# Kernel tuning notes

Measured on AMD Instinct MI355X. Metric: run time of the kernel, lower is better.

Reference implementation:

```python
import jax, jax.numpy as jnp
import numpy as np

N = 200000          # number of nodes (objects)
H = 64              # hidden_size
ARITIES = [1, 2, 3] # arity per relation
NTUP = [250000, 250000, 250000]  # ground atoms per relation


def setup_inputs() -> dict:
    key = jax.random.key(0)
    ks = jax.random.split(key, 32)
    inp = {"node_states": jax.random.normal(ks[0], (N, H), jnp.float32)}
    i = 1
    for r, (a, t) in enumerate(zip(ARITIES, NTUP)):
        inp[f"rel{r}_idx"] = jax.random.randint(ks[i], (t * a,), 0, N, dtype=jnp.int32).astype(jnp.int64); i += 1
        d = a * H
        s = (2.0 / d) ** 0.5
        inp[f"w1_r{r}"] = jax.random.normal(ks[i], (d, d), jnp.float32) * s; i += 1
        inp[f"b1_r{r}"] = jnp.zeros((d,), jnp.float32)
        inp[f"w2_r{r}"] = jax.random.normal(ks[i], (d, d), jnp.float32) * s; i += 1
        inp[f"b2_r{r}"] = jnp.zeros((d,), jnp.float32)
    su = (1.0 / (2 * H)) ** 0.5
    inp["wu1"] = jax.random.normal(ks[i], (2 * H, 2 * H), jnp.float32) * su; i += 1
    inp["bu1"] = jnp.zeros((2 * H,), jnp.float32)
    inp["wu2"] = jax.random.normal(ks[i], (2 * H, H), jnp.float32) * su
    inp["bu2"] = jnp.zeros((H,), jnp.float32)
    return inp


def reference(node_states, rel0_idx, rel1_idx, rel2_idx,
              w1_r0, b1_r0, w2_r0, b2_r0,
              w1_r1, b1_r1, w2_r1, b2_r1,
              w1_r2, b1_r2, w2_r2, b2_r2,
              wu1, bu1, wu2, bu2):
    sum_msg = jnp.zeros_like(node_states)
    rels = [(ARITIES[0], rel0_idx, w1_r0, b1_r0, w2_r0, b2_r0),
            (ARITIES[1], rel1_idx, w1_r1, b1_r1, w2_r1, b2_r1),
            (ARITIES[2], rel2_idx, w1_r2, b1_r2, w2_r2, b2_r2)]
    for a, idx, w1, b1, w2, b2 in rels:
        # gather node states for each ground atom: [T, a*H]
        x = node_states[idx].reshape(-1, a * H)
        h = jax.nn.relu(x @ w1 + b1)
        msg = (h @ w2 + b2).reshape(-1, H)  # [T*a, H]
        # scatter-add messages back to their nodes
        sum_msg = sum_msg.at[idx].add(msg)
    z = jnp.concatenate([sum_msg, node_states], axis=1)  # [N, 2H]
    return jax.nn.relu(z @ wu1 + bu1) @ wu2 + bu2
```

## Files before the change

kernel.cpp:

```cpp
#include <hip/hip_runtime.h>

#define H 64

typedef __attribute__((ext_vector_type(8))) __bf16 bf16x8;
typedef __attribute__((ext_vector_type(4))) float f32x4;
typedef unsigned short u16;
typedef unsigned int u32;

union F8 { bf16x8 b; u16 u[8]; uint4 q; };

__device__ __forceinline__ u16 f2bf(float f) {
    union { __bf16 h; u16 u; } v; v.h = (__bf16)f; return v.u;
}
__device__ __forceinline__ float bf2f(u16 x) {
    return __uint_as_float((u32)x << 16);
}
__device__ __forceinline__ unsigned swz(int col, int k, int K) {
    return ((unsigned)(col * K + k) * 2u) ^ (((unsigned)col & 7u) << 4);
}

struct Seg { const float* src; unsigned dstBytes; int K; int N; };
struct Segs { Seg s[8]; };

__global__ __launch_bounds__(256) void conv_weights(Segs segs, char* out) {
    Seg sg = segs.s[blockIdx.y];
    int total = sg.K * sg.N;
    char* dst = out + sg.dstBytes;
    for (int e = blockIdx.x * 256 + threadIdx.x; e < total; e += gridDim.x * 256) {
        int k = e / sg.N, n = e % sg.N;
        *(u16*)(dst + swz(n, k, sg.K)) = f2bf(sg.src[e]);
    }
}

struct Prep {
    const float4* src; ushort4* dst; int n4;
    const int* idx[3]; int m[3];
    u32* cnt; u32* pos;
};

__global__ __launch_bounds__(256) void conv_nodes_rank(Prep a) {
    const int M01   = a.m[0] + a.m[1];
    const int total = a.n4 + M01 + a.m[2];
    for (int e = blockIdx.x * 256 + threadIdx.x; e < total; e += gridDim.x * 256) {
        if (e < a.n4) {
            float4 f = a.src[e];
            ushort4 o;
            o.x = f2bf(f.x); o.y = f2bf(f.y); o.z = f2bf(f.z); o.w = f2bf(f.w);
            a.dst[e] = o;
        } else {
            const int m = e - a.n4;
            int lm = m, r = 0;
            if (lm >= a.m[0]) {
                lm -= a.m[0]; r = 1;
                if (lm >= a.m[1]) { lm -= a.m[1]; r = 2; }
            }
            a.pos[m] = atomicAdd(a.cnt + a.idx[r][lm], 1u);
        }
    }
}

struct Fix { const int* idx[3]; int m[3]; const u32* base; u32* pos; };

__global__ __launch_bounds__(256) void rank_fix(Fix a) {
    const int total = a.m[0] + a.m[1] + a.m[2];
    for (int e = blockIdx.x * 256 + threadIdx.x; e < total; e += gridDim.x * 256) {
        int lm = e, r = 0;
        if (lm >= a.m[0]) {
            lm -= a.m[0]; r = 1;
            if (lm >= a.m[1]) { lm -= a.m[1]; r = 2; }
        }
        a.pos[e] += a.base[a.idx[r][lm]];
    }
}

__global__ __launch_bounds__(512) void scan_blocks(u32* __restrict__ data,
                                                   u32* __restrict__ sums, int n) {
    __shared__ u32 s[512];
    int tid = threadIdx.x, i = blockIdx.x * 512 + tid;
    u32 v = (i < n) ? data[i] : 0u;
    s[tid] = v; __syncthreads();
    for (int d = 1; d < 512; d <<= 1) {
        u32 t = (tid >= d) ? s[tid - d] : 0u; __syncthreads();
        s[tid] += t; __syncthreads();
    }
    if (i < n) data[i] = s[tid] - v;
    if (tid == 511) sums[blockIdx.x] = s[511];
}

__global__ __launch_bounds__(512) void scan_sums(u32* __restrict__ sums, int nb) {
    __shared__ u32 s[512];
    int tid = threadIdx.x;
    u32 v = (tid < nb) ? sums[tid] : 0u;
    s[tid] = v; __syncthreads();
    for (int d = 1; d < 512; d <<= 1) {
        u32 t = (tid >= d) ? s[tid - d] : 0u; __syncthreads();
        s[tid] += t; __syncthreads();
    }
    if (tid < nb) sums[tid] = s[tid] - v;
}

__global__ __launch_bounds__(512) void scan_add(u32* __restrict__ data,
                                                const u32* __restrict__ sums, int n) {
    int i = blockIdx.x * 512 + threadIdx.x;
    if (i < n) data[i] += sums[blockIdx.x];
}

template<int A>
__global__ __launch_bounds__(512, 4) void msg_kernel(
    const u16* __restrict__ nsb, const int* __restrict__ idx,
    const u32* __restrict__ pos,
    const u16* __restrict__ w1T, const float* __restrict__ b1,
    const u16* __restrict__ w2T, const float* __restrict__ b2,
    u16* __restrict__ msg, int T)
{
    constexpr int D   = A * 64;
    constexpr int KS  = D / 32;
    constexpr int NT  = D / 16;
    constexpr bool DUAL = (A == 1);
    constexpr int WH  = (A == 3) ? 3 : 1;
    constexpr int NTH = NT / WH;
    constexpr int COLH = D / WH;
    constexpr int NPF = (DUAL ? 2 * D * D : COLH * D) / 8 / 512;
    __shared__ __align__(16) u16 Wl[DUAL ? 2 * D * D : COLH * D];
    __shared__ __align__(16) u16 h1[128 * D];

    const int tid  = threadIdx.x;
    const int lane = tid & 63;
    const int w    = tid >> 6;
    const int g    = lane >> 4;
    const int lr   = lane & 15;

    const int tile = blockIdx.x * 128;
    const int trow = tile + w * 16 + lr;
    const int tl   = trow < T ? trow : T - 1;

    auto stage = [&](const u16* gsrc) {
#pragma unroll
        for (int i = 0; i < NPF; ++i) {
            const u16* gp = gsrc + ((i * 512 + tid) << 3);
            u16* lp = Wl + ((i * 512 + (w << 6)) << 3);
            __builtin_amdgcn_global_load_lds(
                (const __attribute__((address_space(1))) void*)gp,
                (__attribute__((address_space(3))) void*)lp, 16, 0, 0);
        }
    };

    int nodes[A];
#pragma unroll
    for (int s = 0; s < A; ++s) nodes[s] = idx[(long)tl * A + s];

    bf16x8 a1[KS];
#pragma unroll
    for (int kk = 0; kk < KS; ++kk) {
        const u16* p = nsb + (long)nodes[kk >> 1] * H + ((kk & 1) * 32 + g * 8);
        F8 t; t.q = *(const uint4*)p;
        a1[kk] = t.b;
    }

    float bias1[NT], bias2[NT];
#pragma unroll
    for (int j = 0; j < NT; ++j) bias1[j] = b1[j * 16 + lr];
#pragma unroll
    for (int j = 0; j < NT; ++j) bias2[j] = b2[j * 16 + lr];

#pragma unroll
    for (int hh = 0; hh < WH; ++hh) {
        stage(DUAL ? w1T : (w1T + (size_t)hh * COLH * D));
        asm volatile("s_waitcnt vmcnt(0)" ::: "memory");
        __syncthreads();

#pragma unroll
        for (int j = 0; j < NTH; ++j) {
            const int jg = hh * NTH + j;
            f32x4 acc = {0.f, 0.f, 0.f, 0.f};
#pragma unroll
            for (int kk = 0; kk < KS; ++kk) {
                F8 bf; bf.q = *(const uint4*)((const char*)Wl + swz(j * 16 + lr, kk * 32 + g * 8, D));
                acc = __builtin_amdgcn_mfma_f32_16x16x32_bf16(a1[kk], bf.b, acc, 0, 0, 0);
            }
#pragma unroll
            for (int r = 0; r < 4; ++r) {
                float vv = acc[r] + bias1[jg];
                vv = vv > 0.f ? vv : 0.f;
                int row = w * 16 + g * 4 + r;
                *(u16*)((char*)h1 + swz(row, jg * 16 + lr, D)) = f2bf(vv);
            }
        }
        if constexpr (!DUAL) __syncthreads();
    }

    bf16x8 a2[KS];
#pragma unroll
    for (int kk = 0; kk < KS; ++kk) {
        int row = w * 16 + lr;
        F8 t; t.q = *(const uint4*)((const char*)h1 + swz(row, kk * 32 + g * 8, D));
        a2[kk] = t.b;
    }

#pragma unroll
    for (int hh = 0; hh < WH; ++hh) {
        if constexpr (!DUAL) {
            stage(w2T + (size_t)hh * COLH * D);
            asm volatile("s_waitcnt vmcnt(0)" ::: "memory");
            __syncthreads();
        }
        const char* W2base = DUAL ? (const char*)(Wl + D * D) : (const char*)Wl;

#pragma unroll
        for (int j = 0; j < NTH; ++j) {
            const int jg = hh * NTH + j;
            f32x4 acc = {0.f, 0.f, 0.f, 0.f};
#pragma unroll
            for (int kk = 0; kk < KS; ++kk) {
                F8 bf; bf.q = *(const uint4*)(W2base + swz(j * 16 + lr, kk * 32 + g * 8, D));
                acc = __builtin_amdgcn_mfma_f32_16x16x32_bf16(a2[kk], bf.b, acc, 0, 0, 0);
            }
            const int gc   = jg * 16 + lr;
            const int slot = gc >> 6;
            const int cs   = gc & 63;
#pragma unroll
            for (int r = 0; r < 4; ++r) {
                int la   = w * 16 + g * 4 + r;
                int mrow = la * A + slot;
                unsigned byte = (((unsigned)(mrow * 64 + cs)) * 2u) ^ (((unsigned)mrow & 7u) << 4);
                *(u16*)((char*)h1 + byte) = f2bf(acc[r] + bias2[jg]);
            }
        }
        if constexpr (!DUAL) { if (hh + 1 < WH) __syncthreads(); }
    }

    const int  mbase = (tile + w * 16) * A;
    const bool full  = (tile + 128 <= T);
#pragma unroll
    for (int i = 0; i < 16 * A; i += 4) {
        int ml   = i + (lane >> 4);
        int mrow = w * 16 * A + ml;
        bool ok  = full || ((tile + w * 16 + ml / A) < T);
        if (ok) {
            u32 p = pos[mbase + ml];
            unsigned byte = (((unsigned)(mrow * 64 + (lane & 15) * 4)) * 2u) ^ (((unsigned)mrow & 7u) << 4);
            uint2 v = *(const uint2*)((const char*)h1 + byte);
            *(uint2*)(msg + (size_t)p * 64 + (lane & 15) * 4) = v;
        }
    }
}

template<int A, bool NSB>
__global__ __launch_bounds__(512) void rel_kernel(
    const float* __restrict__ ns, const u16* __restrict__ nsb,
    const int* __restrict__ idx,
    const u16* __restrict__ w1T, const float* __restrict__ b1,
    const u16* __restrict__ w2T, const float* __restrict__ b2,
    float* __restrict__ dout, int T)
{
    constexpr int D  = A * 64;
    constexpr int KS = D / 32;
    constexpr int NT = D / 16;
    constexpr bool DUAL = (A == 1);
    __shared__ __align__(16) u16 Wl[(DUAL ? 2 : 1) * D * D];
    __shared__ __align__(16) u16 h1[128 * D];

    const int tid  = threadIdx.x;
    const int lane = tid & 63;
    const int w    = tid >> 6;
    const int g    = lane >> 4;
    const int lr   = lane & 15;

    const int tile = blockIdx.x * 128;
    const int trow = tile + w * 16 + lr;
    const int tl   = trow < T ? trow : T - 1;

    {
        constexpr int NV = (DUAL ? 2 : 1) * D * D / 8;
        const uint4* s4 = (const uint4*)w1T;
        uint4* d4 = (uint4*)Wl;
#pragma unroll
        for (int i = 0; i < NV / 512; ++i) d4[i * 512 + tid] = s4[i * 512 + tid];
    }

    int nodes[A];
#pragma unroll
    for (int s = 0; s < A; ++s) nodes[s] = idx[(long)tl * A + s];

    bf16x8 a1[KS];
#pragma unroll
    for (int kk = 0; kk < KS; ++kk) {
        if constexpr (NSB) {
            const u16* p = nsb + (long)nodes[kk >> 1] * H + ((kk & 1) * 32 + g * 8);
            F8 t; t.q = *(const uint4*)p;
            a1[kk] = t.b;
        } else {
            const float* p = ns + (long)nodes[kk >> 1] * H + ((kk & 1) * 32 + g * 8);
            float4 f0 = *(const float4*)p;
            float4 f1 = *(const float4*)(p + 4);
            F8 t;
            t.u[0] = f2bf(f0.x); t.u[1] = f2bf(f0.y); t.u[2] = f2bf(f0.z); t.u[3] = f2bf(f0.w);
            t.u[4] = f2bf(f1.x); t.u[5] = f2bf(f1.y); t.u[6] = f2bf(f1.z); t.u[7] = f2bf(f1.w);
            a1[kk] = t.b;
        }
    }

    float bias1[NT];
#pragma unroll
    for (int j = 0; j < NT; ++j) bias1[j] = b1[j * 16 + lr];

    __syncthreads();

#pragma unroll
    for (int j = 0; j < NT; ++j) {
        f32x4 acc = {0.f, 0.f, 0.f, 0.f};
#pragma unroll
        for (int kk = 0; kk < KS; ++kk) {
            F8 bf; bf.q = *(const uint4*)((const char*)Wl + swz(j * 16 + lr, kk * 32 + g * 8, D));
            acc = __builtin_amdgcn_mfma_f32_16x16x32_bf16(a1[kk], bf.b, acc, 0, 0, 0);
        }
#pragma unroll
        for (int r = 0; r < 4; ++r) {
            float vv = acc[r] + bias1[j];
            vv = vv > 0.f ? vv : 0.f;
            int row = w * 16 + g * 4 + r;
            *(u16*)((char*)h1 + swz(row, j * 16 + lr, D)) = f2bf(vv);
        }
    }

    const char* W2base;
    if constexpr (!DUAL) {
        __syncthreads();
        const uint4* s4 = (const uint4*)w2T;
        uint4* d4 = (uint4*)Wl;
        constexpr int NV = D * D / 8;
#pragma unroll
        for (int i = 0; i < NV / 512; ++i) d4[i * 512 + tid] = s4[i * 512 + tid];
        W2base = (const char*)Wl;
    } else {
        W2base = (const char*)(Wl + D * D);
    }

    bf16x8 a2[KS];
#pragma unroll
    for (int kk = 0; kk < KS; ++kk) {
        int row = w * 16 + lr;
        F8 t; t.q = *(const uint4*)((const char*)h1 + swz(row, kk * 32 + g * 8, D));
        a2[kk] = t.b;
    }

    float bias2[NT];
#pragma unroll
    for (int j = 0; j < NT; ++j) bias2[j] = b2[j * 16 + lr];

    int  nodes2[A][4];
    bool pred[4];
#pragma unroll
    for (int r = 0; r < 4; ++r) {
        int t  = tile + w * 16 + g * 4 + r;
        int tc = t < T ? t : T - 1;
        pred[r] = t < T;
#pragma unroll
        for (int s = 0; s < A; ++s) nodes2[s][r] = idx[(long)tc * A + s];
    }
    if constexpr (!DUAL) __syncthreads();

#pragma unroll
    for (int j = 0; j < NT; ++j) {
        f32x4 acc = {0.f, 0.f, 0.f, 0.f};
#pragma unroll
        for (int kk = 0; kk < KS; ++kk) {
            F8 bf; bf.q = *(const uint4*)(W2base + swz(j * 16 + lr, kk * 32 + g * 8, D));
            acc = __builtin_amdgcn_mfma_f32_16x16x32_bf16(a2[kk], bf.b, acc, 0, 0, 0);
        }
        const int slot = j >> 2;
        const int coff = (j & 3) * 16 + lr;
#pragma unroll
        for (int r = 0; r < 4; ++r) {
            if (pred[r])
                unsafeAtomicAdd(dout + (long)nodes2[slot][r] * H + coff, acc[r] + bias2[j]);
        }
    }
}

template<bool SEG, bool NSB>
__global__ __launch_bounds__(512) void update_kernel(
    const float* __restrict__ ns, const u16* __restrict__ nsb,
    const float* __restrict__ sum,
    const u32* __restrict__ base, const u16* __restrict__ msg, int Mtot,
    const u16* __restrict__ wu1T, const float* __restrict__ bu1,
    const u16* __restrict__ wu2T, const float* __restrict__ bu2,
    float* __restrict__ out, int N)
{
    __shared__ __align__(16) u16 Wl[128 * 128 + 64 * 128];
    __shared__ __align__(16) u16 h[128 * 128];

    const int tid  = threadIdx.x;
    const int lane = tid & 63;
    const int w    = tid >> 6;
    const int g    = lane >> 4;
    const int lr   = lane & 15;

    {
        const uint4* s4 = (const uint4*)wu1T;
        uint4* d4 = (uint4*)Wl;
#pragma unroll
        for (int i = 0; i < 6; ++i) d4[i * 512 + tid] = s4[i * 512 + tid];
    }

    const int tile = blockIdx.x * 128;
    const int trow = tile + w * 16 + lr;
    const int tl   = trow < N ? trow : N - 1;

    bf16x8 a1[4];
    if constexpr (SEG) {
        const u32 s = base[tl];
        const u32 e = (tl + 1 < N) ? base[tl + 1] : (u32)Mtot;
        float s0[8], s1[8];
#pragma unroll
        for (int j = 0; j < 8; ++j) { s0[j] = 0.f; s1[j] = 0.f; }
        for (u32 p = s; p < e; ++p) {
            const u16* row = msg + (size_t)p * 64;
            F8 v0, v1;
            v0.q = *(const uint4*)(row + g * 8);
            v1.q = *(const uint4*)(row + 32 + g * 8);
#pragma unroll
            for (int j = 0; j < 8; ++j) { s0[j] += bf2f(v0.u[j]); s1[j] += bf2f(v1.u[j]); }
        }
        F8 t0, t1;
#pragma unroll
        for (int j = 0; j < 8; ++j) { t0.u[j] = f2bf(s0[j]); t1.u[j] = f2bf(s1[j]); }
        a1[0] = t0.b; a1[1] = t1.b;
    } else {
#pragma unroll
        for (int kk = 0; kk < 2; ++kk) {
            int k = kk * 32 + g * 8;
            const float* p = sum + (long)tl * H + k;
            float4 f0 = *(const float4*)p;
            float4 f1 = *(const float4*)(p + 4);
            F8 t;
            t.u[0] = f2bf(f0.x); t.u[1] = f2bf(f0.y); t.u[2] = f2bf(f0.z); t.u[3] = f2bf(f0.w);
            t.u[4] = f2bf(f1.x); t.u[5] = f2bf(f1.y); t.u[6] = f2bf(f1.z); t.u[7] = f2bf(f1.w);
            a1[kk] = t.b;
        }
    }
#pragma unroll
    for (int kk = 2; kk < 4; ++kk) {
        if (NSB) {
            const u16* prow = nsb + (long)tl * H;
            F8 t; t.q = *(const uint4*)(prow + (kk - 2) * 32 + g * 8);
            a1[kk] = t.b;
        } else {
            int k = (kk - 2) * 32 + g * 8;
            const float* p = ns + (long)tl * H + k;
            float4 f0 = *(const float4*)p;
            float4 f1 = *(const float4*)(p + 4);
            F8 t;
            t.u[0] = f2bf(f0.x); t.u[1] = f2bf(f0.y); t.u[2] = f2bf(f0.z); t.u[3] = f2bf(f0.w);
            t.u[4] = f2bf(f1.x); t.u[5] = f2bf(f1.y); t.u[6] = f2bf(f1.z); t.u[7] = f2bf(f1.w);
            a1[kk] = t.b;
        }
    }

    float bias1[8], bias2[4];
#pragma unroll
    for (int j = 0; j < 8; ++j) bias1[j] = bu1[j * 16 + lr];
#pragma unroll
    for (int j = 0; j < 4; ++j) bias2[j] = bu2[j * 16 + lr];

    __syncthreads();

#pragma unroll
    for (int j = 0; j < 8; ++j) {
        f32x4 acc = {0.f, 0.f, 0.f, 0.f};
#pragma unroll
        for (int kk = 0; kk < 4; ++kk) {
            F8 bf; bf.q = *(const uint4*)((const char*)Wl + swz(j * 16 + lr, kk * 32 + g * 8, 128));
            acc = __builtin_amdgcn_mfma_f32_16x16x32_bf16(a1[kk], bf.b, acc, 0, 0, 0);
        }
#pragma unroll
        for (int r = 0; r < 4; ++r) {
            float vv = acc[r] + bias1[j];
            vv = vv > 0.f ? vv : 0.f;
            int row = w * 16 + g * 4 + r;
            *(u16*)((char*)h + swz(row, j * 16 + lr, 128)) = f2bf(vv);
        }
    }

    bf16x8 a2[4];
#pragma unroll
    for (int kk = 0; kk < 4; ++kk) {
        int row = w * 16 + lr;
        F8 t; t.q = *(const uint4*)((const char*)h + swz(row, kk * 32 + g * 8, 128));
        a2[kk] = t.b;
    }

    const char* W2base = (const char*)(Wl + 128 * 128);
#pragma unroll
    for (int j = 0; j < 4; ++j) {
        f32x4 acc = {0.f, 0.f, 0.f, 0.f};
#pragma unroll
        for (int kk = 0; kk < 4; ++kk) {
            F8 bf; bf.q = *(const uint4*)(W2base + swz(j * 16 + lr, kk * 32 + g * 8, 128));
            acc = __builtin_amdgcn_mfma_f32_16x16x32_bf16(a2[kk], bf.b, acc, 0, 0, 0);
        }
#pragma unroll
        for (int r = 0; r < 4; ++r) {
            int t = tile + w * 16 + g * 4 + r;
            if (t < N) out[(long)t * H + j * 16 + lr] = acc[r] + bias2[j];
        }
    }
}

extern "C" void kernel_launch(void* const* d_in, const int* in_sizes, int n_in,
                              void* d_out, int out_size, void* d_ws, size_t ws_size,
                              hipStream_t stream) {
    const float* ns = (const float*)d_in[0];
    const int* idxs[3] = { (const int*)d_in[1], (const int*)d_in[6], (const int*)d_in[11] };
    const float* b1s[3] = { (const float*)d_in[3], (const float*)d_in[8], (const float*)d_in[13] };
    const float* b2s[3] = { (const float*)d_in[5], (const float*)d_in[10], (const float*)d_in[15] };
    const float* bu1 = (const float*)d_in[17];
    const float* bu2 = (const float*)d_in[19];

    const int N = in_sizes[0] / H;
    const int Ts[3] = { in_sizes[1], in_sizes[6] / 2, in_sizes[11] / 3 };
    const int Ms[3] = { Ts[0] * 1, Ts[1] * 2, Ts[2] * 3 };
    const long Mtot = (long)Ms[0] + Ms[1] + Ms[2];

    char* wsb = (char*)d_ws;
    auto AL = [](size_t x) { return (x + 255) & ~(size_t)255; };

    const unsigned O_W1R0 = 0;
    const unsigned O_W2R0 = O_W1R0 + 64 * 64 * 2;
    const unsigned O_W1R1 = O_W2R0 + 64 * 64 * 2;
    const unsigned O_W2R1 = O_W1R1 + 128 * 128 * 2;
    const unsigned O_W1R2 = O_W2R1 + 128 * 128 * 2;
    const unsigned O_W2R2 = O_W1R2 + 192 * 192 * 2;
    const unsigned O_WU1  = O_W2R2 + 192 * 192 * 2;
    const unsigned O_WU2  = O_WU1 + 128 * 128 * 2;
    const size_t  wEnd    = O_WU2 + 128 * 64 * 2;
    const unsigned wOff1[3] = { O_W1R0, O_W1R1, O_W1R2 };
    const unsigned wOff2[3] = { O_W2R0, O_W2R1, O_W2R2 };

    const int nb = (N + 511) / 512;

    const size_t O_CNT = AL(wEnd);
    const size_t O_SUM = AL(O_CNT + (size_t)N * 4);
    const size_t O_POS = AL(O_SUM + (size_t)nb * 4);
    const size_t O_NSB = AL(O_POS + (size_t)Mtot * 4);
    const size_t nsLen = (size_t)N * H * 2;
    const size_t O_MSG = AL(O_NSB + nsLen);
    const size_t need  = O_MSG + (size_t)Mtot * 128;

    const bool sorted = (nb <= 512) && (ws_size >= need);
    const bool nsbOk  = ws_size >= O_NSB + nsLen;

    Segs segs;
    segs.s[0] = {(const float*)d_in[2],  O_W1R0, 64, 64};
    segs.s[1] = {(const float*)d_in[4],  O_W2R0, 64, 64};
    segs.s[2] = {(const float*)d_in[7],  O_W1R1, 128, 128};
    segs.s[3] = {(const float*)d_in[9],  O_W2R1, 128, 128};
    segs.s[4] = {(const float*)d_in[12], O_W1R2, 192, 192};
    segs.s[5] = {(const float*)d_in[14], O_W2R2, 192, 192};
    segs.s[6] = {(const float*)d_in[16], O_WU1, 128, 128};
    segs.s[7] = {(const float*)d_in[18], O_WU2, 128, 64};

    conv_weights<<<dim3(36, 8), 256, 0, stream>>>(segs, wsb);

    float* dout = (float*)d_out;
    u16* nsbp = (u16*)(wsb + O_NSB);

    const u16* W1[3] = { (const u16*)(wsb + wOff1[0]), (const u16*)(wsb + wOff1[1]), (const u16*)(wsb + wOff1[2]) };
    const u16* W2[3] = { (const u16*)(wsb + wOff2[0]), (const u16*)(wsb + wOff2[1]), (const u16*)(wsb + wOff2[2]) };

    auto gT = [](int T) { return (T + 127) / 128; };

    if (sorted) {
        u32* cnt = (u32*)(wsb + O_CNT);
        u32* sums = (u32*)(wsb + O_SUM);
        u32* pos = (u32*)(wsb + O_POS);
        u16* msg = (u16*)(wsb + O_MSG);

        hipMemsetAsync(cnt, 0, (size_t)N * 4, stream);

        Prep pp;
        pp.src = (const float4*)ns; pp.dst = (ushort4*)nsbp; pp.n4 = N * H / 4;
        for (int r = 0; r < 3; ++r) { pp.idx[r] = idxs[r]; pp.m[r] = Ms[r]; }
        pp.cnt = cnt; pp.pos = pos;
        conv_nodes_rank<<<2048, 256, 0, stream>>>(pp);

        scan_blocks<<<nb, 512, 0, stream>>>(cnt, sums, N);
        scan_sums<<<1, 512, 0, stream>>>(sums, nb);
        scan_add<<<nb, 512, 0, stream>>>(cnt, sums, N);

        Fix fx;
        for (int r = 0; r < 3; ++r) { fx.idx[r] = idxs[r]; fx.m[r] = Ms[r]; }
        fx.base = cnt; fx.pos = pos;
        rank_fix<<<2048, 256, 0, stream>>>(fx);

        msg_kernel<1><<<gT(Ts[0]), 512, 0, stream>>>(
            nsbp, idxs[0], pos, W1[0], b1s[0], W2[0], b2s[0], msg, Ts[0]);
        msg_kernel<2><<<gT(Ts[1]), 512, 0, stream>>>(
            nsbp, idxs[1], pos + Ms[0], W1[1], b1s[1], W2[1], b2s[1], msg, Ts[1]);
        msg_kernel<3><<<gT(Ts[2]), 512, 0, stream>>>(
            nsbp, idxs[2], pos + Ms[0] + Ms[1], W1[2], b1s[2], W2[2], b2s[2], msg, Ts[2]);

        update_kernel<true, true><<<(N + 127) / 128, 512, 0, stream>>>(
            ns, nsbp, nullptr, cnt, msg, (int)Mtot,
            (const u16*)(wsb + O_WU1), bu1, (const u16*)(wsb + O_WU2), bu2, dout, N);
    } else {
        if (nsbOk) {
            Prep pp;
            pp.src = (const float4*)ns; pp.dst = (ushort4*)nsbp; pp.n4 = N * H / 4;
            for (int r = 0; r < 3; ++r) { pp.idx[r] = idxs[0]; pp.m[r] = 0; }
            pp.cnt = (u32*)(wsb + O_CNT); pp.pos = (u32*)(wsb + O_CNT);
            conv_nodes_rank<<<512, 256, 0, stream>>>(pp);
        }
        hipMemsetAsync(dout, 0, (size_t)N * H * sizeof(float), stream);
        for (int r = 0; r < 3; ++r) {
            const int T = Ts[r], nbl = gT(T);
            if (nsbOk) {
                if (r == 0) rel_kernel<1, true><<<nbl, 512, 0, stream>>>(ns, nsbp, idxs[0], W1[0], b1s[0], W2[0], b2s[0], dout, T);
                if (r == 1) rel_kernel<2, true><<<nbl, 512, 0, stream>>>(ns, nsbp, idxs[1], W1[1], b1s[1], W2[1], b2s[1], dout, T);
                if (r == 2) rel_kernel<3, true><<<nbl, 512, 0, stream>>>(ns, nsbp, idxs[2], W1[2], b1s[2], W2[2], b2s[2], dout, T);
            } else {
                if (r == 0) rel_kernel<1, false><<<nbl, 512, 0, stream>>>(ns, nullptr, idxs[0], W1[0], b1s[0], W2[0], b2s[0], dout, T);
                if (r == 1) rel_kernel<2, false><<<nbl, 512, 0, stream>>>(ns, nullptr, idxs[1], W1[1], b1s[1], W2[1], b2s[1], dout, T);
                if (r == 2) rel_kernel<3, false><<<nbl, 512, 0, stream>>>(ns, nullptr, idxs[2], W1[2], b1s[2], W2[2], b2s[2], dout, T);
            }
        }
        if (nsbOk)
            update_kernel<false, true><<<(N + 127) / 128, 512, 0, stream>>>(
                ns, nsbp, dout, nullptr, nullptr, 0,
                (const u16*)(wsb + O_WU1), bu1, (const u16*)(wsb + O_WU2), bu2, dout, N);
        else
            update_kernel<false, false><<<(N + 127) / 128, 512, 0, stream>>>(
                ns, nullptr, dout, nullptr, nullptr, 0,
                (const u16*)(wsb + O_WU1), bu1, (const u16*)(wsb + O_WU2), bu2, dout, N);
    }
}
```

Before: 302.4 us.

## Fuse rank counting and message MLPs into one mega kernel with order-indirection

Merges the atomic rank-counting pass and the three per-relation message MLP kernels into a single launch. Rank blocks are striped among the message blocks so the atomics overlap with the matrix work. Messages are now written in original atom order, and a new ord_fix kernel builds a sorted permutation that the update kernel reads indirectly. The bf16 node-state copy is dropped, so gathers read fp32 and convert in registers. The cost is an extra indirection in the segmented reduction and more gather bandwidth from fp32 reads.

```diff
diff --git a/kernel.cpp b/kernel.cpp
--- a/kernel.cpp
+++ b/kernel.cpp
@@ -29,47 +29,6 @@
     for (int e = blockIdx.x * 256 + threadIdx.x; e < total; e += gridDim.x * 256) {
         int k = e / sg.N, n = e % sg.N;
         *(u16*)(dst + swz(n, k, sg.K)) = f2bf(sg.src[e]);
-    }
-}
-
-struct Prep {
-    const float4* src; ushort4* dst; int n4;
-    const int* idx[3]; int m[3];
-    u32* cnt; u32* pos;
-};
-
-__global__ __launch_bounds__(256) void conv_nodes_rank(Prep a) {
-    const int M01   = a.m[0] + a.m[1];
-    const int total = a.n4 + M01 + a.m[2];
-    for (int e = blockIdx.x * 256 + threadIdx.x; e < total; e += gridDim.x * 256) {
-        if (e < a.n4) {
-            float4 f = a.src[e];
-            ushort4 o;
-            o.x = f2bf(f.x); o.y = f2bf(f.y); o.z = f2bf(f.z); o.w = f2bf(f.w);
-            a.dst[e] = o;
-        } else {
-            const int m = e - a.n4;
-            int lm = m, r = 0;
-            if (lm >= a.m[0]) {
-                lm -= a.m[0]; r = 1;
-                if (lm >= a.m[1]) { lm -= a.m[1]; r = 2; }
-            }
-            a.pos[m] = atomicAdd(a.cnt + a.idx[r][lm], 1u);
-        }
-    }
-}
-
-struct Fix { const int* idx[3]; int m[3]; const u32* base; u32* pos; };
-
-__global__ __launch_bounds__(256) void rank_fix(Fix a) {
-    const int total = a.m[0] + a.m[1] + a.m[2];
-    for (int e = blockIdx.x * 256 + threadIdx.x; e < total; e += gridDim.x * 256) {
-        int lm = e, r = 0;
-        if (lm >= a.m[0]) {
-            lm -= a.m[0]; r = 1;
-            if (lm >= a.m[1]) { lm -= a.m[1]; r = 2; }
-        }
-        a.pos[e] += a.base[a.idx[r][lm]];
     }
 }
 
@@ -105,13 +64,28 @@
     if (i < n) data[i] += sums[blockIdx.x];
 }
 
+struct OFix {
+    const int* idx0; const int* idx1; const int* idx2;
+    int m0, m1, m2;
+    const u32* base; const u32* pre; u32* ord;
+};
+
+__global__ __launch_bounds__(256) void ord_fix(OFix a) {
+    const int Mtot = a.m0 + a.m1 + a.m2;
+    for (int e = blockIdx.x * 256 + threadIdx.x; e < Mtot; e += gridDim.x * 256) {
+        int lm = e, node;
+        if (lm < a.m0) node = a.idx0[lm];
+        else { lm -= a.m0; if (lm < a.m1) node = a.idx1[lm]; else node = a.idx2[lm - a.m1]; }
+        a.ord[a.base[node] + a.pre[e]] = (u32)e;
+    }
+}
+
 template<int A>
-__global__ __launch_bounds__(512, 4) void msg_kernel(
-    const u16* __restrict__ nsb, const int* __restrict__ idx,
-    const u32* __restrict__ pos,
+__device__ __forceinline__ void msg_body(
+    const float* __restrict__ ns, const int* __restrict__ idx,
     const u16* __restrict__ w1T, const float* __restrict__ b1,
     const u16* __restrict__ w2T, const float* __restrict__ b2,
-    u16* __restrict__ msg, int T)
+    u16* __restrict__ msgR, int T, int bid, u16* Wl, u16* h1)
 {
     constexpr int D   = A * 64;
     constexpr int KS  = D / 32;
@@ -121,8 +95,6 @@
     constexpr int NTH = NT / WH;
     constexpr int COLH = D / WH;
     constexpr int NPF = (DUAL ? 2 * D * D : COLH * D) / 8 / 512;
-    __shared__ __align__(16) u16 Wl[DUAL ? 2 * D * D : COLH * D];
-    __shared__ __align__(16) u16 h1[128 * D];
 
     const int tid  = threadIdx.x;
     const int lane = tid & 63;
@@ -130,7 +102,7 @@
     const int g    = lane >> 4;
     const int lr   = lane & 15;
 
-    const int tile = blockIdx.x * 128;
+    const int tile = bid * 128;
     const int trow = tile + w * 16 + lr;
     const int tl   = trow < T ? trow : T - 1;
 
@@ -152,8 +124,12 @@
     bf16x8 a1[KS];
 #pragma unroll
     for (int kk = 0; kk < KS; ++kk) {
-        const u16* p = nsb + (long)nodes[kk >> 1] * H + ((kk & 1) * 32 + g * 8);
-        F8 t; t.q = *(const uint4*)p;
+        const float* p = ns + (long)nodes[kk >> 1] * H + ((kk & 1) * 32 + g * 8);
+        float4 f0 = *(const float4*)p;
+        float4 f1 = *(const float4*)(p + 4);
+        F8 t;
+        t.u[0] = f2bf(f0.x); t.u[1] = f2bf(f0.y); t.u[2] = f2bf(f0.z); t.u[3] = f2bf(f0.w);
+        t.u[4] = f2bf(f1.x); t.u[5] = f2bf(f1.y); t.u[6] = f2bf(f1.z); t.u[7] = f2bf(f1.w);
         a1[kk] = t.b;
     }
 
@@ -237,18 +213,66 @@
         int mrow = w * 16 * A + ml;
         bool ok  = full || ((tile + w * 16 + ml / A) < T);
         if (ok) {
-            u32 p = pos[mbase + ml];
             unsigned byte = (((unsigned)(mrow * 64 + (lane & 15) * 4)) * 2u) ^ (((unsigned)mrow & 7u) << 4);
             uint2 v = *(const uint2*)((const char*)h1 + byte);
-            *(uint2*)(msg + (size_t)p * 64 + (lane & 15) * 4) = v;
-        }
-    }
-}
-
-template<int A, bool NSB>
+            *(uint2*)(msgR + (size_t)(mbase + ml) * 64 + (lane & 15) * 4) = v;
+        }
+    }
+}
+
+struct MegaA {
+    const float* ns;
+    const int* idx0; const int* idx1; const int* idx2;
+    int m0, m1, m2, t0, t1, t2;
+    u32* cnt; u32* pre;
+    const u16 *w10, *w20, *w11, *w21, *w12, *w22;
+    const float *b10, *b20, *b11, *b21, *b12, *b22;
+    u16* msgu;
+    int nrank, nb2, nb1, nb0, striped;
+};
+
+__global__ __launch_bounds__(512, 4) void mega_kernel(MegaA a) {
+    __shared__ __align__(16) u16 sm[36864];
+    const int bx = blockIdx.x;
+    int kind, id;
+    if (a.striped) {
+        const int strip = 4 * a.nrank;
+        if (bx < strip) {
+            if ((bx & 3) == 3) { kind = 1; id = bx >> 2; }
+            else               { kind = 0; id = bx - (bx >> 2); }
+        } else { kind = 0; id = bx - a.nrank; }
+    } else {
+        if (bx < a.nrank) { kind = 1; id = bx; }
+        else              { kind = 0; id = bx - a.nrank; }
+    }
+
+    if (kind == 1) {
+        const int Mtot = a.m0 + a.m1 + a.m2;
+        for (int e = id * 512 + (int)threadIdx.x; e < Mtot; e += a.nrank * 512) {
+            int lm = e, node;
+            if (lm < a.m0) node = a.idx0[lm];
+            else { lm -= a.m0; if (lm < a.m1) node = a.idx1[lm]; else node = a.idx2[lm - a.m1]; }
+            a.pre[e] = atomicAdd(a.cnt + node, 1u);
+        }
+        return;
+    }
+
+    const int nmsg = a.nb2 + a.nb1 + a.nb0;
+    if (id >= nmsg) return;
+    if (id < a.nb2)
+        msg_body<3>(a.ns, a.idx2, a.w12, a.b12, a.w22, a.b22,
+                    a.msgu + (size_t)(a.m0 + a.m1) * 64, a.t2, id, sm, sm + 12288);
+    else if (id < a.nb2 + a.nb1)
+        msg_body<2>(a.ns, a.idx1, a.w11, a.b11, a.w21, a.b21,
+                    a.msgu + (size_t)a.m0 * 64, a.t1, id - a.nb2, sm, sm + 16384);
+    else
+        msg_body<1>(a.ns, a.idx0, a.w10, a.b10, a.w20, a.b20,
+                    a.msgu, a.t0, id - a.nb2 - a.nb1, sm, sm + 8192);
+}
+
+template<int A>
 __global__ __launch_bounds__(512) void rel_kernel(
-    const float* __restrict__ ns, const u16* __restrict__ nsb,
-    const int* __restrict__ idx,
+    const float* __restrict__ ns, const int* __restrict__ idx,
     const u16* __restrict__ w1T, const float* __restrict__ b1,
     const u16* __restrict__ w2T, const float* __restrict__ b2,
     float* __restrict__ dout, int T)
@@ -285,19 +309,13 @@
     bf16x8 a1[KS];
 #pragma unroll
     for (int kk = 0; kk < KS; ++kk) {
-        if constexpr (NSB) {
-            const u16* p = nsb + (long)nodes[kk >> 1] * H + ((kk & 1) * 32 + g * 8);
-            F8 t; t.q = *(const uint4*)p;
-            a1[kk] = t.b;
-        } else {
-            const float* p = ns + (long)nodes[kk >> 1] * H + ((kk & 1) * 32 + g * 8);
-            float4 f0 = *(const float4*)p;
-            float4 f1 = *(const float4*)(p + 4);
-            F8 t;
-            t.u[0] = f2bf(f0.x); t.u[1] = f2bf(f0.y); t.u[2] = f2bf(f0.z); t.u[3] = f2bf(f0.w);
-            t.u[4] = f2bf(f1.x); t.u[5] = f2bf(f1.y); t.u[6] = f2bf(f1.z); t.u[7] = f2bf(f1.w);
-            a1[kk] = t.b;
-        }
+        const float* p = ns + (long)nodes[kk >> 1] * H + ((kk & 1) * 32 + g * 8);
+        float4 f0 = *(const float4*)p;
+        float4 f1 = *(const float4*)(p + 4);
+        F8 t;
+        t.u[0] = f2bf(f0.x); t.u[1] = f2bf(f0.y); t.u[2] = f2bf(f0.z); t.u[3] = f2bf(f0.w);
+        t.u[4] = f2bf(f1.x); t.u[5] = f2bf(f1.y); t.u[6] = f2bf(f1.z); t.u[7] = f2bf(f1.w);
+        a1[kk] = t.b;
     }
 
     float bias1[NT];
@@ -378,11 +396,11 @@
     }
 }
 
-template<bool SEG, bool NSB>
+template<bool SEG>
 __global__ __launch_bounds__(512) void update_kernel(
-    const float* __restrict__ ns, const u16* __restrict__ nsb,
-    const float* __restrict__ sum,
-    const u32* __restrict__ base, const u16* __restrict__ msg, int Mtot,
+    const float* __restrict__ ns, const float* __restrict__ sum,
+    const u32* __restrict__ ord, const u32* __restrict__ base,
+    const u16* __restrict__ msg, int Mtot,
     const u16* __restrict__ wu1T, const float* __restrict__ bu1,
     const u16* __restrict__ wu2T, const float* __restrict__ bu2,
     float* __restrict__ out, int N)
@@ -415,7 +433,7 @@
 #pragma unroll
         for (int j = 0; j < 8; ++j) { s0[j] = 0.f; s1[j] = 0.f; }
         for (u32 p = s; p < e; ++p) {
-            const u16* row = msg + (size_t)p * 64;
+            const u16* row = msg + (size_t)ord[p] * 64;
             F8 v0, v1;
             v0.q = *(const uint4*)(row + g * 8);
             v1.q = *(const uint4*)(row + 32 + g * 8);
@@ -441,20 +459,14 @@
     }
 #pragma unroll
     for (int kk = 2; kk < 4; ++kk) {
-        if (NSB) {
-            const u16* prow = nsb + (long)tl * H;
-            F8 t; t.q = *(const uint4*)(prow + (kk - 2) * 32 + g * 8);
-            a1[kk] = t.b;
-        } else {
-            int k = (kk - 2) * 32 + g * 8;
-            const float* p = ns + (long)tl * H + k;
-            float4 f0 = *(const float4*)p;
-            float4 f1 = *(const float4*)(p + 4);
-            F8 t;
-            t.u[0] = f2bf(f0.x); t.u[1] = f2bf(f0.y); t.u[2] = f2bf(f0.z); t.u[3] = f2bf(f0.w);
-            t.u[4] = f2bf(f1.x); t.u[5] = f2bf(f1.y); t.u[6] = f2bf(f1.z); t.u[7] = f2bf(f1.w);
-            a1[kk] = t.b;
-        }
+        int k = (kk - 2) * 32 + g * 8;
+        const float* p = ns + (long)tl * H + k;
+        float4 f0 = *(const float4*)p;
+        float4 f1 = *(const float4*)(p + 4);
+        F8 t;
+        t.u[0] = f2bf(f0.x); t.u[1] = f2bf(f0.y); t.u[2] = f2bf(f0.z); t.u[3] = f2bf(f0.w);
+        t.u[4] = f2bf(f1.x); t.u[5] = f2bf(f1.y); t.u[6] = f2bf(f1.z); t.u[7] = f2bf(f1.w);
+        a1[kk] = t.b;
     }
 
     float bias1[8], bias2[4];
@@ -541,14 +553,12 @@
 
     const size_t O_CNT = AL(wEnd);
     const size_t O_SUM = AL(O_CNT + (size_t)N * 4);
-    const size_t O_POS = AL(O_SUM + (size_t)nb * 4);
-    const size_t O_NSB = AL(O_POS + (size_t)Mtot * 4);
-    const size_t nsLen = (size_t)N * H * 2;
-    const size_t O_MSG = AL(O_NSB + nsLen);
+    const size_t O_PRE = AL(O_SUM + (size_t)nb * 4);
+    const size_t O_ORD = AL(O_PRE + (size_t)Mtot * 4);
+    const size_t O_MSG = AL(O_ORD + (size_t)Mtot * 4);
     const size_t need  = O_MSG + (size_t)Mtot * 128;
 
     const bool sorted = (nb <= 512) && (ws_size >= need);
-    const bool nsbOk  = ws_size >= O_NSB + nsLen;
 
     Segs segs;
     segs.s[0] = {(const float*)d_in[2],  O_W1R0, 64, 64};
@@ -560,11 +570,7 @@
     segs.s[6] = {(const float*)d_in[16], O_WU1, 128, 128};
     segs.s[7] = {(const float*)d_in[18], O_WU2, 128, 64};
 
-    conv_weights<<<dim3(36, 8), 256, 0, stream>>>(segs, wsb);
-
     float* dout = (float*)d_out;
-    u16* nsbp = (u16*)(wsb + O_NSB);
-
     const u16* W1[3] = { (const u16*)(wsb + wOff1[0]), (const u16*)(wsb + wOff1[1]), (const u16*)(wsb + wOff1[2]) };
     const u16* W2[3] = { (const u16*)(wsb + wOff2[0]), (const u16*)(wsb + wOff2[1]), (const u16*)(wsb + wOff2[2]) };
 
@@ -573,64 +579,59 @@
     if (sorted) {
         u32* cnt = (u32*)(wsb + O_CNT);
         u32* sums = (u32*)(wsb + O_SUM);
-        u32* pos = (u32*)(wsb + O_POS);
-        u16* msg = (u16*)(wsb + O_MSG);
+        u32* pre = (u32*)(wsb + O_PRE);
+        u32* ord = (u32*)(wsb + O_ORD);
+        u16* msgu = (u16*)(wsb + O_MSG);
 
         hipMemsetAsync(cnt, 0, (size_t)N * 4, stream);
-
-        Prep pp;
-        pp.src = (const float4*)ns; pp.dst = (ushort4*)nsbp; pp.n4 = N * H / 4;
-        for (int r = 0; r < 3; ++r) { pp.idx[r] = idxs[r]; pp.m[r] = Ms[r]; }
-        pp.cnt = cnt; pp.pos = pos;
-        conv_nodes_rank<<<2048, 256, 0, stream>>>(pp);
+        conv_weights<<<dim3(36, 8), 256, 0, stream>>>(segs, wsb);
+
+        const int nb0 = gT(Ts[0]), nb1 = gT(Ts[1]), nb2 = gT(Ts[2]);
+        const int nmsg = nb0 + nb1 + nb2;
+        int NR = nmsg / 3; if (NR > 1024) NR = 1024; if (NR < 1) NR = 1;
+        const int striped = (nmsg >= 3 * NR) ? 1 : 0;
+        const int NTOT = NR + nmsg;
+
+        MegaA ma;
+        ma.ns = ns;
+        ma.idx0 = idxs[0]; ma.idx1 = idxs[1]; ma.idx2 = idxs[2];
+        ma.m0 = Ms[0]; ma.m1 = Ms[1]; ma.m2 = Ms[2];
+        ma.t0 = Ts[0]; ma.t1 = Ts[1]; ma.t2 = Ts[2];
+        ma.cnt = cnt; ma.pre = pre;
+        ma.w10 = W1[0]; ma.w20 = W2[0];
+        ma.w11 = W1[1]; ma.w21 = W2[1];
+        ma.w12 = W1[2]; ma.w22 = W2[2];
+        ma.b10 = b1s[0]; ma.b20 = b2s[0];
+        ma.b11 = b1s[1]; ma.b21 = b2s[1];
+        ma.b12 = b1s[2]; ma.b22 = b2s[2];
+        ma.msgu = msgu;
+        ma.nrank = NR; ma.nb2 = nb2; ma.nb1 = nb1; ma.nb0 = nb0; ma.striped = striped;
+        mega_kernel<<<NTOT, 512, 0, stream>>>(ma);
 
         scan_blocks<<<nb, 512, 0, stream>>>(cnt, sums, N);
         scan_sums<<<1, 512, 0, stream>>>(sums, nb);
         scan_add<<<nb, 512, 0, stream>>>(cnt, sums, N);
 
-        Fix fx;
-        for (int r = 0; r < 3; ++r) { fx.idx[r] = idxs[r]; fx.m[r] = Ms[r]; }
-        fx.base = cnt; fx.pos = pos;
-        rank_fix<<<2048, 256, 0, stream>>>(fx);
-
-        msg_kernel<1><<<gT(Ts[0]), 512, 0, stream>>>(
-            nsbp, idxs[0], pos, W1[0], b1s[0], W2[0], b2s[0], msg, Ts[0]);
-        msg_kernel<2><<<gT(Ts[1]), 512, 0, stream>>>(
-            nsbp, idxs[1], pos + Ms[0], W1[1], b1s[1], W2[1], b2s[1], msg, Ts[1]);
-        msg_kernel<3><<<gT(Ts[2]), 512, 0, stream>>>(
-            nsbp, idxs[2], pos + Ms[0] + Ms[1], W1[2], b1s[2], W2[2], b2s[2], msg, Ts[2]);
-
-        update_kernel<true, true><<<(N + 127) / 128, 512, 0, stream>>>(
-            ns, nsbp, nullptr, cnt, msg, (int)Mtot,
+        OFix fx;
+        fx.idx0 = idxs[0]; fx.idx1 = idxs[1]; fx.idx2 = idxs[2];
+        fx.m0 = Ms[0]; fx.m1 = Ms[1]; fx.m2 = Ms[2];
+        fx.base = cnt; fx.pre = pre; fx.ord = ord;
+        ord_fix<<<2048, 256, 0, stream>>>(fx);
+
+        update_kernel<true><<<(N + 127) / 128, 512, 0, stream>>>(
+            ns, nullptr, ord, cnt, msgu, (int)Mtot,
             (const u16*)(wsb + O_WU1), bu1, (const u16*)(wsb + O_WU2), bu2, dout, N);
     } else {
-        if (nsbOk) {
-            Prep pp;
-            pp.src = (const float4*)ns; pp.dst = (ushort4*)nsbp; pp.n4 = N * H / 4;
-            for (int r = 0; r < 3; ++r) { pp.idx[r] = idxs[0]; pp.m[r] = 0; }
-            pp.cnt = (u32*)(wsb + O_CNT); pp.pos = (u32*)(wsb + O_CNT);
-            conv_nodes_rank<<<512, 256, 0, stream>>>(pp);
-        }
+        conv_weights<<<dim3(36, 8), 256, 0, stream>>>(segs, wsb);
         hipMemsetAsync(dout, 0, (size_t)N * H * sizeof(float), stream);
         for (int r = 0; r < 3; ++r) {
             const int T = Ts[r], nbl = gT(T);
-            if (nsbOk) {
-                if (r == 0) rel_kernel<1, true><<<nbl, 512, 0, stream>>>(ns, nsbp, idxs[0], W1[0], b1s[0], W2[0], b2s[0], dout, T);
-                if (r == 1) rel_kernel<2, true><<<nbl, 512, 0, stream>>>(ns, nsbp, idxs[1], W1[1], b1s[1], W2[1], b2s[1], dout, T);
-                if (r == 2) rel_kernel<3, true><<<nbl, 512, 0, stream>>>(ns, nsbp, idxs[2], W1[2], b1s[2], W2[2], b2s[2], dout, T);
-            } else {
-                if (r == 0) rel_kernel<1, false><<<nbl, 512, 0, stream>>>(ns, nullptr, idxs[0], W1[0], b1s[0], W2[0], b2s[0], dout, T);
-                if (r == 1) rel_kernel<2, false><<<nbl, 512, 0, stream>>>(ns, nullptr, idxs[1], W1[1], b1s[1], W2[1], b2s[1], dout, T);
-                if (r == 2) rel_kernel<3, false><<<nbl, 512, 0, stream>>>(ns, nullptr, idxs[2], W1[2], b1s[2], W2[2], b2s[2], dout, T);
-            }
-        }
-        if (nsbOk)
-            update_kernel<false, true><<<(N + 127) / 128, 512, 0, stream>>>(
-                ns, nsbp, dout, nullptr, nullptr, 0,
-                (const u16*)(wsb + O_WU1), bu1, (const u16*)(wsb + O_WU2), bu2, dout, N);
-        else
-            update_kernel<false, false><<<(N + 127) / 128, 512, 0, stream>>>(
-                ns, nullptr, dout, nullptr, nullptr, 0,
-                (const u16*)(wsb + O_WU1), bu1, (const u16*)(wsb + O_WU2), bu2, dout, N);
-    }
-}
+            if (r == 0) rel_kernel<1><<<nbl, 512, 0, stream>>>(ns, idxs[0], W1[0], b1s[0], W2[0], b2s[0], dout, T);
+            if (r == 1) rel_kernel<2><<<nbl, 512, 0, stream>>>(ns, idxs[1], W1[1], b1s[1], W2[1], b2s[1], dout, T);
+            if (r == 2) rel_kernel<3><<<nbl, 512, 0, stream>>>(ns, idxs[2], W1[2], b1s[2], W2[2], b2s[2], dout, T);
+        }
+        update_kernel<false><<<(N + 127) / 128, 512, 0, stream>>>(
+            ns, dout, nullptr, nullptr, nullptr, 0,
+            (const u16*)(wsb + O_WU1), bu1, (const u16*)(wsb + O_WU2), bu2, dout, N);
+    }
+}
```

Result: no change. 300.0 us (-0.8%).
